# Performance work log

Measured on AMD Instinct MI355X. Metric: run time of the kernel, lower is better.

The kernel has to match this reference:

```python
import jax, jax.numpy as jnp
import numpy as np

N_NODES, N_EDGES, F_IN = 8192, 32768, 16
N_SUB, N_GRAPH = 512, 32
EDGE_DIM, HID = 5, 128
DIMS = [(16, 32), (32, 64), (64, 64)]  # (M_in, M_out) per NNConv layer


def _segment_mean(x, seg, n):
    s = jax.ops.segment_sum(x, seg, num_segments=n)
    c = jax.ops.segment_sum(jnp.ones((x.shape[0], 1), x.dtype), seg, num_segments=n)
    return s / jnp.maximum(c, 1.0)


def _nnconv(x, src, dst, eattr, W1, b1, W2, b2, root, bias):
    # edge MLP -> per-edge weight matrix theta: [E, M_in, M_out]
    h = jax.nn.relu(eattr @ W1 + b1)
    theta = (h @ W2 + b2).reshape(-1, x.shape[1], root.shape[1])
    msg = jnp.einsum('ei,eio->eo', x[src], theta)          # gather + per-edge matvec
    agg = jax.ops.segment_sum(msg, dst, num_segments=x.shape[0])  # scatter-add (aggr='add')
    return agg + x @ root + bias


def setup_inputs() -> dict:
    key = jax.random.key(0)
    ks = jax.random.split(key, 32)
    inp = {}
    inp['x'] = jax.random.normal(ks[0], (N_NODES, F_IN), jnp.float32)
    inp['edge_index'] = jax.random.randint(ks[1], (2, N_EDGES), 0, N_NODES)
    inp['edge_attr'] = jax.random.uniform(ks[2], (N_EDGES, EDGE_DIM), jnp.float32)
    inp['node_to_subgraph'] = jnp.sort(jax.random.randint(ks[3], (N_NODES,), 0, N_SUB))
    inp['subgraph_to_graph'] = jnp.sort(jax.random.randint(ks[4], (N_SUB,), 0, N_GRAPH))
    i = 5
    for l, (ci, co) in enumerate(DIMS):
        inp[f'W1_{l}'] = jax.random.normal(ks[i], (EDGE_DIM, HID), jnp.float32) * 0.1
        inp[f'b1_{l}'] = jnp.zeros((HID,), jnp.float32)
        inp[f'W2_{l}'] = jax.random.normal(ks[i + 1], (HID, ci * co), jnp.float32) * 0.05
        inp[f'b2_{l}'] = jnp.zeros((ci * co,), jnp.float32)
        inp[f'root_{l}'] = jax.random.normal(ks[i + 2], (ci, co), jnp.float32) * 0.1
        inp[f'bias_{l}'] = jnp.zeros((co,), jnp.float32)
        i += 3
    inp['fc1_w'] = jax.random.normal(ks[i], (64, 32), jnp.float32) * 0.1
    inp['fc1_b'] = jnp.zeros((32,), jnp.float32)
    inp['fc2_w'] = jax.random.normal(ks[i + 1], (32, 16), jnp.float32) * 0.1
    inp['fc2_b'] = jnp.zeros((16,), jnp.float32)
    inp['fc3_w'] = jax.random.normal(ks[i + 2], (16, 1), jnp.float32) * 0.1
    inp['fc3_b'] = jnp.zeros((1,), jnp.float32)
    return inp


def reference(x, edge_index, edge_attr, node_to_subgraph, subgraph_to_graph,
              W1_0, b1_0, W2_0, b2_0, root_0, bias_0,
              W1_1, b1_1, W2_1, b2_1, root_1, bias_1,
              W1_2, b1_2, W2_2, b2_2, root_2, bias_2,
              fc1_w, fc1_b, fc2_w, fc2_b, fc3_w, fc3_b):
    src, dst = edge_index[0], edge_index[1]
    layers = [(W1_0, b1_0, W2_0, b2_0, root_0, bias_0),
              (W1_1, b1_1, W2_1, b2_1, root_1, bias_1),
              (W1_2, b1_2, W2_2, b2_2, root_2, bias_2)]
    h = x
    for (W1, b1, W2, b2, root, bias) in layers:
        h = jax.nn.elu(_nnconv(h, src, dst, edge_attr, W1, b1, W2, b2, root, bias))
    h = _segment_mean(h, node_to_subgraph, N_SUB)      # global_mean_pool over subgraphs
    h = _segment_mean(h, subgraph_to_graph, N_GRAPH)   # global_mean_pool over graphs
    h = jax.nn.elu(h @ fc1_w + fc1_b)
    h = jax.nn.elu(h @ fc2_w + fc2_b)
    return (h @ fc3_w + fc3_b).reshape(-1)
```

## Files before the change

kernel.cpp:

```cpp
#include <hip/hip_runtime.h>

#define E_EDGES 32768
#define NN 8192
#define HID 128
#define KS 4

typedef _Float16 half8 __attribute__((ext_vector_type(8)));
typedef _Float16 half4 __attribute__((ext_vector_type(4)));
typedef float f32x4 __attribute__((ext_vector_type(4)));

__global__ void zero_init_k(int* __restrict__ hist, float* __restrict__ pools, int npool) {
  int t = blockIdx.x * 256 + threadIdx.x;
  if (t < NN) hist[t] = 0;
  if (t < npool) pools[t] = 0.f;
}

__global__ void hist_k(const int* __restrict__ dst, int* __restrict__ hist) {
  int e = blockIdx.x * 256 + threadIdx.x;
  if (e < E_EDGES) atomicAdd(&hist[dst[e]], 1);
}

__global__ void scan_k(const int* __restrict__ hist, int* __restrict__ roff, int* __restrict__ cursor) {
  __shared__ int ps[1024];
  int t = threadIdx.x;
  int loc[8]; int s = 0;
  int base = t * 8;
#pragma unroll
  for (int j = 0; j < 8; ++j) { loc[j] = s; s += hist[base + j]; }
  ps[t] = s;
  __syncthreads();
  for (int off = 1; off < 1024; off <<= 1) {
    int v = 0;
    if (t >= off) v = ps[t - off];
    __syncthreads();
    if (t >= off) ps[t] += v;
    __syncthreads();
  }
  int excl = (t == 0) ? 0 : ps[t - 1];
#pragma unroll
  for (int j = 0; j < 8; ++j) { int v = excl + loc[j]; roff[base + j] = v; cursor[base + j] = v; }
  if (t == 1023) roff[NN] = ps[1023];
}

__global__ void scatter_k(const int* __restrict__ dst, int* __restrict__ cursor, int* __restrict__ eidx) {
  int e = blockIdx.x * 256 + threadIdx.x;
  if (e < E_EDGES) { int p = atomicAdd(&cursor[dst[e]], 1); eidx[p] = e; }
}

template <int CI, int CO>
__device__ inline void prep_b_one(int idx, const float* __restrict__ W2,
                                  const float* __restrict__ b2, _Float16* __restrict__ out) {
  constexpr int Kmain = 128 * CI;
  constexpr int FC = CO / 16;
  int j = idx & 7;
  int h8 = idx >> 3;
  int lane = h8 & 63;
  int quad = lane >> 4, l15 = lane & 15;
  int rest = h8 >> 6;
  int fc = rest & (FC - 1);
  int c = rest / FC;
  int k = c * 32 + quad * 8 + j;
  int n = fc * 16 + l15;
  float v = 0.f;
  if (k < Kmain) v = W2[(size_t)k * CO + n];
  else if (k < Kmain + CI) v = b2[(k - Kmain) * CO + n];
  out[idx] = (_Float16)v;
}

__global__ void prep_b_all_k(const float* __restrict__ W2_0, const float* __restrict__ b2_0, _Float16* __restrict__ o0,
                             const float* __restrict__ W2_1, const float* __restrict__ b2_1, _Float16* __restrict__ o1,
                             const float* __restrict__ W2_2, const float* __restrict__ b2_2, _Float16* __restrict__ o2) {
  constexpr int N0 = 2176 * 32;
  constexpr int N1 = 4224 * 64;
  constexpr int N2 = 8320 * 64;
  int idx = blockIdx.x * 256 + threadIdx.x;
  if (idx < N0) prep_b_one<16, 32>(idx, W2_0, b2_0, o0);
  else if (idx < N0 + N1) prep_b_one<32, 64>(idx - N0, W2_1, b2_1, o1);
  else if (idx < N0 + N1 + N2) prep_b_one<64, 64>(idx - N0 - N1, W2_2, b2_2, o2);
}

__device__ inline half8 pack8(float4 a, float4 b) {
  half8 r;
  r[0] = (_Float16)a.x; r[1] = (_Float16)a.y; r[2] = (_Float16)a.z; r[3] = (_Float16)a.w;
  r[4] = (_Float16)b.x; r[5] = (_Float16)b.y; r[6] = (_Float16)b.z; r[7] = (_Float16)b.w;
  return r;
}

__device__ __forceinline__ void gload_lds16(const _Float16* g, _Float16* l) {
  __builtin_amdgcn_global_load_lds(
      (__attribute__((address_space(1))) void*)(size_t)(const void*)g,
      (__attribute__((address_space(3))) void*)(size_t)(void*)l, 16, 0, 0);
}

template <int CI, int CO>
__launch_bounds__(256, 2)
__global__ void msg_mfma_k(const float* __restrict__ xcur, const int* __restrict__ src,
                           const float* __restrict__ eattr, const float* __restrict__ W1,
                           const float* __restrict__ b1, const _Float16* __restrict__ Bsw,
                           float* __restrict__ msgbuf) {
  constexpr int ME = 256;
  constexpr int HSTR = 36;
  constexpr int FC = CO / 16;
  constexpr int NMAIN = CI / 4;
  constexpr int XPN = (CI == 64) ? 2 : 1;
  constexpr int RHALF = 4 * FC * 64 * 8;

  __shared__ _Float16 he_s[ME * HSTR];
  __shared__ float ea_s[ME * 5];
  __shared__ float W1s[5 * 32];
  __shared__ float b1s[32];
  __shared__ int src_s[ME];
  __shared__ _Float16 bls[2 * RHALF];

  int t = threadIdx.x;
  int e0 = blockIdx.x * ME;
  int y = blockIdx.y;
  int hbeg = y * 32;

  for (int j = t; j < ME * 5; j += 256) ea_s[j] = eattr[e0 * 5 + j];
  if (t < 5 * 32) W1s[t] = W1[(t >> 5) * HID + hbeg + (t & 31)];
  if (t < 32) b1s[t] = b1[hbeg + t];
  src_s[t] = src[e0 + t];
  __syncthreads();

  for (int j = t; j < 32 * ME; j += 256) {
    int hl = j & 31, e = j >> 5;
    float v = b1s[hl];
#pragma unroll
    for (int d = 0; d < 5; ++d) v += ea_s[e * 5 + d] * W1s[d * 32 + hl];
    he_s[e * HSTR + hl] = (_Float16)fmaxf(v, 0.f);
  }
  __syncthreads();

  int lane = t & 63;
  int w = t >> 6;
  int quad = lane >> 4, l15 = lane & 15;
  int qsh = (quad >> 1) << 4;
  int Rg0 = y * NMAIN;
  int NR = NMAIN + ((y == 3) ? 1 : 0);

  half8 xp[4][XPN];
  const _Float16* hbp[4];
#pragma unroll
  for (int fr = 0; fr < 4; ++fr) {
    int e = w * 64 + fr * 16 + l15;
    const float* xr = xcur + (size_t)src_s[e] * CI;
    int i0 = (CI == 16) ? ((quad & 1) * 8) : (quad * 8);
    float4 v0 = *(const float4*)(xr + i0);
    float4 v1 = *(const float4*)(xr + i0 + 4);
    xp[fr][0] = pack8(v0, v1);
    if constexpr (CI == 64) {
      float4 v2 = *(const float4*)(xr + i0 + 32);
      float4 v3 = *(const float4*)(xr + i0 + 36);
      xp[fr][1] = pack8(v2, v3);
    }
    hbp[fr] = he_s + e * HSTR;
  }

  f32x4 acc[4][FC];
#pragma unroll
  for (int fr = 0; fr < 4; ++fr)
#pragma unroll
    for (int fc = 0; fc < FC; ++fc)
#pragma unroll
      for (int r = 0; r < 4; ++r) acc[fr][fc][r] = 0.f;

  auto stageR = [&](int rg, int buf) {
    const _Float16* gb = Bsw + (size_t)rg * RHALF + w * (FC * 512);
    _Float16* lb = bls + buf * RHALF + w * (FC * 512);
#pragma unroll
    for (int i = 0; i < FC; ++i)
      gload_lds16(gb + i * 512 + lane * 8, lb + i * 512);
  };

  stageR(Rg0, 0);
  stageR(Rg0 + 1, 1);

  for (int r = 0; r < NR; ++r) {
    if (r + 1 < NR) {
      if constexpr (FC == 4) asm volatile("s_waitcnt vmcnt(4)" ::: "memory");
      else                   asm volatile("s_waitcnt vmcnt(2)" ::: "memory");
    } else {
      asm volatile("s_waitcnt vmcnt(0)" ::: "memory");
    }
    __builtin_amdgcn_s_barrier();

    const _Float16* bp = bls + (r & 1) * RHALF;
    int c0 = (Rg0 + r) * 4;

    if (r < NMAIN) {
      unsigned int hp2[4];
      half4 hp4[4];
      if constexpr (CI == 64) {
        int oh = (c0 >> 1) - hbeg;
#pragma unroll
        for (int fr = 0; fr < 4; ++fr) hp2[fr] = *(const unsigned int*)(hbp[fr] + oh);
      } else if constexpr (CI == 32) {
        int oh = c0 - hbeg;
#pragma unroll
        for (int fr = 0; fr < 4; ++fr) hp4[fr] = *(const half4*)(hbp[fr] + oh);
      }
#pragma unroll
      for (int cr = 0; cr < 4; ++cr) {
        int c = c0 + cr;
        half8 a[4];
#pragma unroll
        for (int fr = 0; fr < 4; ++fr) {
          if constexpr (CI == 64) {
            unsigned short hb = (unsigned short)((cr >= 2) ? (hp2[fr] >> 16) : hp2[fr]);
            _Float16 hv = __builtin_bit_cast(_Float16, hb);
            a[fr] = xp[fr][cr & 1] * hv;
          } else if constexpr (CI == 32) {
            a[fr] = xp[fr][0] * hp4[fr][cr];
          } else {
            unsigned int hw = *(const unsigned int*)(hbp[fr] + (2 * c - hbeg));
            _Float16 hv = __builtin_bit_cast(_Float16, (unsigned short)(hw >> qsh));
            a[fr] = xp[fr][0] * hv;
          }
        }
#pragma unroll
        for (int fc = 0; fc < FC; ++fc) {
          half8 bf = *(const half8*)&bp[((cr * FC + fc) * 64 + lane) * 8];
#pragma unroll
          for (int fr = 0; fr < 4; ++fr)
            acc[fr][fc] = __builtin_amdgcn_mfma_f32_16x16x32_f16(a[fr], bf, acc[fr][fc], 0, 0, 0);
        }
      }
    } else {
#pragma unroll
      for (int cr = 0; cr < 4; ++cr) {
        half8 a[4];
#pragma unroll
        for (int fr = 0; fr < 4; ++fr) a[fr] = xp[fr][(CI == 64) ? (cr & 1) : 0];
#pragma unroll
        for (int fc = 0; fc < FC; ++fc) {
          half8 bf = *(const half8*)&bp[((cr * FC + fc) * 64 + lane) * 8];
#pragma unroll
          for (int fr = 0; fr < 4; ++fr)
            acc[fr][fc] = __builtin_amdgcn_mfma_f32_16x16x32_f16(a[fr], bf, acc[fr][fc], 0, 0, 0);
        }
      }
    }

    asm volatile("s_waitcnt lgkmcnt(0)" ::: "memory");
    __builtin_amdgcn_s_barrier();
    if (r + 2 < NR) stageR(Rg0 + r + 2, r & 1);
  }

  float* mb = msgbuf + ((size_t)y * E_EDGES + e0) * CO;
#pragma unroll
  for (int fr = 0; fr < 4; ++fr)
#pragma unroll
    for (int fc = 0; fc < FC; ++fc)
#pragma unroll
      for (int r = 0; r < 4; ++r) {
        int el = w * 64 + fr * 16 + quad * 4 + r;
        int o = fc * 16 + l15;
        mb[el * CO + o] = acc[fr][fc][r];
      }
}

template <int CI, int CO, bool POOL>
__global__ void gather_elu_k(const float* __restrict__ xcur, const float* __restrict__ root,
                             const float* __restrict__ bias, const float* __restrict__ msgbuf,
                             const int* __restrict__ roff, const int* __restrict__ eidx,
                             float* __restrict__ xnext, const int* __restrict__ n2s,
                             float* __restrict__ ssum, float* __restrict__ scnt) {
  constexpr int NB = 256 / CO;
  __shared__ float xs[NB * CI];
  int t = threadIdx.x;
  int n0 = blockIdx.x * NB;
  for (int j = t; j < NB * CI; j += 256) xs[j] = xcur[n0 * CI + j];
  __syncthreads();
  int nl = t / CO, o = t & (CO - 1);
  int n = n0 + nl;
  float a = bias[o];
#pragma unroll
  for (int i = 0; i < CI; ++i) a += xs[nl * CI + i] * root[i * CO + o];
  int j1 = roff[n + 1];
  for (int j = roff[n]; j < j1; ++j) {
    int e = eidx[j];
    float m = 0.f;
#pragma unroll
    for (int s = 0; s < KS; ++s) m += msgbuf[((size_t)s * E_EDGES + e) * CO + o];
    a += m;
  }
  float v = a > 0.f ? a : expm1f(a);
  if constexpr (POOL) {
    int s = n2s[n];
    atomicAdd(&ssum[(s << 6) + o], v);
    if (o == 0) atomicAdd(&scnt[s], 1.f);
  } else {
    xnext[n * CO + o] = v;
  }
}

__global__ void pg_head_k(const float* __restrict__ ssum, const float* __restrict__ scnt,
                          const int* __restrict__ s2g,
                          const float* __restrict__ w1, const float* __restrict__ b1,
                          const float* __restrict__ w2, const float* __restrict__ b2,
                          const float* __restrict__ w3, const float* __restrict__ b3,
                          float* __restrict__ out) {
  int g = blockIdx.x;
  int t = threadIdx.x;
  __shared__ int s2s[512];
  __shared__ float hm[64], h1[32], h2[16];
  for (int i = t; i < 512; i += 64) s2s[i] = s2g[i];
  __syncthreads();
  float acc = 0.f, cnt = 0.f;
  for (int s = 0; s < 512; ++s) {
    if (s2s[s] == g) {
      acc += ssum[(s << 6) + t] / fmaxf(scnt[s], 1.f);
      cnt += 1.f;
    }
  }
  hm[t] = acc / fmaxf(cnt, 1.f);
  __syncthreads();
  if (t < 32) {
    float a = b1[t];
    for (int i = 0; i < 64; ++i) a += hm[i] * w1[i * 32 + t];
    h1[t] = a > 0.f ? a : expm1f(a);
  }
  __syncthreads();
  if (t < 16) {
    float a = b2[t];
    for (int i = 0; i < 32; ++i) a += h1[i] * w2[i * 16 + t];
    h2[t] = a > 0.f ? a : expm1f(a);
  }
  __syncthreads();
  if (t == 0) {
    float a = b3[0];
    for (int i = 0; i < 16; ++i) a += h2[i] * w3[i];
    out[g] = a;
  }
}

extern "C" void kernel_launch(void* const* d_in, const int* in_sizes, int n_in,
                              void* d_out, int out_size, void* d_ws, size_t ws_size,
                              hipStream_t stream) {
  (void)in_sizes; (void)n_in; (void)out_size; (void)ws_size;
  const float* x0 = (const float*)d_in[0];
  const int* ei = (const int*)d_in[1];
  const float* ea = (const float*)d_in[2];
  const int* n2s = (const int*)d_in[3];
  const int* s2g = (const int*)d_in[4];
  const float* W1_[3] = {(const float*)d_in[5], (const float*)d_in[11], (const float*)d_in[17]};
  const float* b1_[3] = {(const float*)d_in[6], (const float*)d_in[12], (const float*)d_in[18]};
  const float* W2_[3] = {(const float*)d_in[7], (const float*)d_in[13], (const float*)d_in[19]};
  const float* b2_[3] = {(const float*)d_in[8], (const float*)d_in[14], (const float*)d_in[20]};
  const float* rt_[3] = {(const float*)d_in[9], (const float*)d_in[15], (const float*)d_in[21]};
  const float* bs_[3] = {(const float*)d_in[10], (const float*)d_in[16], (const float*)d_in[22]};
  const float* fc1w = (const float*)d_in[23]; const float* fc1b = (const float*)d_in[24];
  const float* fc2w = (const float*)d_in[25]; const float* fc2b = (const float*)d_in[26];
  const float* fc3w = (const float*)d_in[27]; const float* fc3b = (const float*)d_in[28];
  float* out = (float*)d_out;

  const int* srcp = ei;
  const int* dstp = ei + E_EDGES;

  char* wsb = (char*)d_ws;
  size_t off = 0;
  auto alloc = [&](size_t bytes) {
    void* p = wsb + off;
    off += (bytes + 255) & ~(size_t)255;
    return p;
  };
  _Float16* Bsw0 = (_Float16*)alloc((size_t)2176 * 32 * 2);
  _Float16* Bsw1 = (_Float16*)alloc((size_t)4224 * 64 * 2);
  _Float16* Bsw2 = (_Float16*)alloc((size_t)8320 * 64 * 2);
  float* msgbuf = (float*)alloc((size_t)KS * E_EDGES * 64 * 4);
  float* x1 = (float*)alloc((size_t)NN * 32 * 4);
  float* x2 = (float*)alloc((size_t)NN * 64 * 4);
  int* hist = (int*)alloc((size_t)NN * 4);
  int* roff = (int*)alloc((size_t)(NN + 1) * 4);
  int* cursor = (int*)alloc((size_t)NN * 4);
  int* eidx = (int*)alloc((size_t)E_EDGES * 4);
  const int npool = 512 * 64 + 512;
  float* pools = (float*)alloc((size_t)npool * 4);
  float* ssum = pools;
  float* scnt = pools + 512 * 64;

  zero_init_k<<<(npool + 255) / 256, 256, 0, stream>>>(hist, pools, npool);
  hist_k<<<E_EDGES / 256, 256, 0, stream>>>(dstp, hist);
  scan_k<<<1, 1024, 0, stream>>>(hist, roff, cursor);
  scatter_k<<<E_EDGES / 256, 256, 0, stream>>>(dstp, cursor, eidx);
  prep_b_all_k<<<(2176 * 32 + 4224 * 64 + 8320 * 64) / 256, 256, 0, stream>>>(
      W2_[0], b2_[0], Bsw0, W2_[1], b2_[1], Bsw1, W2_[2], b2_[2], Bsw2);

  dim3 mg(E_EDGES / 256, KS);
  msg_mfma_k<16, 32><<<mg, 256, 0, stream>>>(x0, srcp, ea, W1_[0], b1_[0], Bsw0, msgbuf);
  gather_elu_k<16, 32, false><<<NN / 8, 256, 0, stream>>>(x0, rt_[0], bs_[0], msgbuf, roff, eidx, x1, nullptr, nullptr, nullptr);
  msg_mfma_k<32, 64><<<mg, 256, 0, stream>>>(x1, srcp, ea, W1_[1], b1_[1], Bsw1, msgbuf);
  gather_elu_k<32, 64, false><<<NN / 4, 256, 0, stream>>>(x1, rt_[1], bs_[1], msgbuf, roff, eidx, x2, nullptr, nullptr, nullptr);
  msg_mfma_k<64, 64><<<mg, 256, 0, stream>>>(x2, srcp, ea, W1_[2], b1_[2], Bsw2, msgbuf);
  gather_elu_k<64, 64, true><<<NN / 4, 256, 0, stream>>>(x2, rt_[2], bs_[2], msgbuf, roff, eidx, nullptr, n2s, ssum, scnt);

  pg_head_k<<<32, 64, 0, stream>>>(ssum, scnt, s2g, fc1w, fc1b, fc2w, fc2b, fc3w, fc3b, out);
}
```

Measured before the change: 278.3 us.

## Fuse zero-init into prep, shuffle scan, re-split MFMA waves, vectorize gather

Merges the buffer-zeroing kernel into the weight-swizzle prep kernel, which now writes eight halves per thread, and replaces the shared-memory Hillis-Steele scan with a wave-shuffle scan. Re-partitions the MFMA message kernel so each wave covers 128 edges and half of the output columns instead of 64 edges and all columns. This halves the LDS B-fragment reads per MFMA at the cost of more accumulator registers. The gather/ELU kernel now handles four outputs per thread with float4 loads and stores, cutting launch count and memory instructions.

```diff
diff --git a/kernel.cpp b/kernel.cpp
--- a/kernel.cpp
+++ b/kernel.cpp
@@ -9,37 +9,41 @@
 typedef _Float16 half4 __attribute__((ext_vector_type(4)));
 typedef float f32x4 __attribute__((ext_vector_type(4)));
 
-__global__ void zero_init_k(int* __restrict__ hist, float* __restrict__ pools, int npool) {
-  int t = blockIdx.x * 256 + threadIdx.x;
-  if (t < NN) hist[t] = 0;
-  if (t < npool) pools[t] = 0.f;
-}
-
 __global__ void hist_k(const int* __restrict__ dst, int* __restrict__ hist) {
   int e = blockIdx.x * 256 + threadIdx.x;
   if (e < E_EDGES) atomicAdd(&hist[dst[e]], 1);
 }
 
 __global__ void scan_k(const int* __restrict__ hist, int* __restrict__ roff, int* __restrict__ cursor) {
-  __shared__ int ps[1024];
+  __shared__ int wsum[16];
   int t = threadIdx.x;
+  int lane = t & 63, wv = t >> 6;
+  int base = t * 8;
   int loc[8]; int s = 0;
-  int base = t * 8;
 #pragma unroll
   for (int j = 0; j < 8; ++j) { loc[j] = s; s += hist[base + j]; }
-  ps[t] = s;
-  __syncthreads();
-  for (int off = 1; off < 1024; off <<= 1) {
-    int v = 0;
-    if (t >= off) v = ps[t - off];
-    __syncthreads();
-    if (t >= off) ps[t] += v;
-    __syncthreads();
-  }
-  int excl = (t == 0) ? 0 : ps[t - 1];
+  int inc = s;
+#pragma unroll
+  for (int off = 1; off < 64; off <<= 1) {
+    int u = __shfl_up(inc, off, 64);
+    if (lane >= off) inc += u;
+  }
+  if (lane == 63) wsum[wv] = inc;
+  __syncthreads();
+  if (t < 64) {
+    int u = (t < 16) ? wsum[t] : 0;
+#pragma unroll
+    for (int off = 1; off < 16; off <<= 1) {
+      int x = __shfl_up(u, off, 64);
+      if (lane >= off) u += x;
+    }
+    if (t < 16) wsum[t] = u;
+  }
+  __syncthreads();
+  int excl = (wv ? wsum[wv - 1] : 0) + inc - s;
 #pragma unroll
   for (int j = 0; j < 8; ++j) { int v = excl + loc[j]; roff[base + j] = v; cursor[base + j] = v; }
-  if (t == 1023) roff[NN] = ps[1023];
+  if (t == 1023) roff[NN] = wsum[15];
 }
 
 __global__ void scatter_k(const int* __restrict__ dst, int* __restrict__ cursor, int* __restrict__ eidx) {
@@ -48,35 +52,45 @@
 }
 
 template <int CI, int CO>
-__device__ inline void prep_b_one(int idx, const float* __restrict__ W2,
-                                  const float* __restrict__ b2, _Float16* __restrict__ out) {
+__device__ inline void prep8(int h8, const float* __restrict__ W2,
+                             const float* __restrict__ b2, _Float16* __restrict__ out) {
   constexpr int Kmain = 128 * CI;
   constexpr int FC = CO / 16;
-  int j = idx & 7;
-  int h8 = idx >> 3;
   int lane = h8 & 63;
   int quad = lane >> 4, l15 = lane & 15;
   int rest = h8 >> 6;
   int fc = rest & (FC - 1);
   int c = rest / FC;
-  int k = c * 32 + quad * 8 + j;
+  int k0 = c * 32 + quad * 8;
   int n = fc * 16 + l15;
-  float v = 0.f;
-  if (k < Kmain) v = W2[(size_t)k * CO + n];
-  else if (k < Kmain + CI) v = b2[(k - Kmain) * CO + n];
-  out[idx] = (_Float16)v;
-}
-
-__global__ void prep_b_all_k(const float* __restrict__ W2_0, const float* __restrict__ b2_0, _Float16* __restrict__ o0,
-                             const float* __restrict__ W2_1, const float* __restrict__ b2_1, _Float16* __restrict__ o1,
-                             const float* __restrict__ W2_2, const float* __restrict__ b2_2, _Float16* __restrict__ o2) {
-  constexpr int N0 = 2176 * 32;
-  constexpr int N1 = 4224 * 64;
-  constexpr int N2 = 8320 * 64;
-  int idx = blockIdx.x * 256 + threadIdx.x;
-  if (idx < N0) prep_b_one<16, 32>(idx, W2_0, b2_0, o0);
-  else if (idx < N0 + N1) prep_b_one<32, 64>(idx - N0, W2_1, b2_1, o1);
-  else if (idx < N0 + N1 + N2) prep_b_one<64, 64>(idx - N0 - N1, W2_2, b2_2, o2);
+  half8 r;
+#pragma unroll
+  for (int j = 0; j < 8; ++j) {
+    int k = k0 + j;
+    float v = 0.f;
+    if (k < Kmain) v = W2[(size_t)k * CO + n];
+    else if (k < Kmain + CI) v = b2[(k - Kmain) * CO + n];
+    r[j] = (_Float16)v;
+  }
+  *(half8*)(out + (size_t)h8 * 8) = r;
+}
+
+__global__ void prep_zero_k(const float* __restrict__ W2_0, const float* __restrict__ b2_0, _Float16* __restrict__ o0,
+                            const float* __restrict__ W2_1, const float* __restrict__ b2_1, _Float16* __restrict__ o1,
+                            const float* __restrict__ W2_2, const float* __restrict__ b2_2, _Float16* __restrict__ o2,
+                            int4* __restrict__ hist4, float4* __restrict__ pools4) {
+  constexpr int H0 = 2176 * 32 / 8;
+  constexpr int H1 = 4224 * 64 / 8;
+  constexpr int H2 = 8320 * 64 / 8;
+  constexpr int HT = H0 + H1 + H2;
+  constexpr int ZH = NN / 4;
+  constexpr int ZP = (512 * 64 + 512) / 4;
+  int tid = blockIdx.x * 256 + threadIdx.x;
+  if (tid < H0) prep8<16, 32>(tid, W2_0, b2_0, o0);
+  else if (tid < H0 + H1) prep8<32, 64>(tid - H0, W2_1, b2_1, o1);
+  else if (tid < HT) prep8<64, 64>(tid - H0 - H1, W2_2, b2_2, o2);
+  else if (tid < HT + ZH) hist4[tid - HT] = int4{0, 0, 0, 0};
+  else if (tid < HT + ZH + ZP) pools4[tid - HT - ZH] = float4{0.f, 0.f, 0.f, 0.f};
 }
 
 __device__ inline half8 pack8(float4 a, float4 b) {
@@ -101,6 +115,8 @@
   constexpr int ME = 256;
   constexpr int HSTR = 36;
   constexpr int FC = CO / 16;
+  constexpr int FCW = FC / 2;
+  constexpr int FR = 8;
   constexpr int NMAIN = CI / 4;
   constexpr int XPN = (CI == 64) ? 2 : 1;
   constexpr int RHALF = 4 * FC * 64 * 8;
@@ -134,16 +150,17 @@
 
   int lane = t & 63;
   int w = t >> 6;
+  int we = w & 1, wn = w >> 1;
   int quad = lane >> 4, l15 = lane & 15;
   int qsh = (quad >> 1) << 4;
   int Rg0 = y * NMAIN;
   int NR = NMAIN + ((y == 3) ? 1 : 0);
 
-  half8 xp[4][XPN];
-  const _Float16* hbp[4];
-#pragma unroll
-  for (int fr = 0; fr < 4; ++fr) {
-    int e = w * 64 + fr * 16 + l15;
+  half8 xp[FR][XPN];
+  int hoff[FR];
+#pragma unroll
+  for (int fr = 0; fr < FR; ++fr) {
+    int e = we * 128 + fr * 16 + l15;
     const float* xr = xcur + (size_t)src_s[e] * CI;
     int i0 = (CI == 16) ? ((quad & 1) * 8) : (quad * 8);
     float4 v0 = *(const float4*)(xr + i0);
@@ -154,14 +171,14 @@
       float4 v3 = *(const float4*)(xr + i0 + 36);
       xp[fr][1] = pack8(v2, v3);
     }
-    hbp[fr] = he_s + e * HSTR;
-  }
-
-  f32x4 acc[4][FC];
-#pragma unroll
-  for (int fr = 0; fr < 4; ++fr)
-#pragma unroll
-    for (int fc = 0; fc < FC; ++fc)
+    hoff[fr] = e * HSTR;
+  }
+
+  f32x4 acc[FR][FCW];
+#pragma unroll
+  for (int fr = 0; fr < FR; ++fr)
+#pragma unroll
+    for (int fc = 0; fc < FCW; ++fc)
 #pragma unroll
       for (int r = 0; r < 4; ++r) acc[fr][fc][r] = 0.f;
 
@@ -189,23 +206,23 @@
     int c0 = (Rg0 + r) * 4;
 
     if (r < NMAIN) {
-      unsigned int hp2[4];
-      half4 hp4[4];
+      unsigned int hp2[FR];
+      half4 hp4[FR];
       if constexpr (CI == 64) {
         int oh = (c0 >> 1) - hbeg;
 #pragma unroll
-        for (int fr = 0; fr < 4; ++fr) hp2[fr] = *(const unsigned int*)(hbp[fr] + oh);
+        for (int fr = 0; fr < FR; ++fr) hp2[fr] = *(const unsigned int*)(he_s + hoff[fr] + oh);
       } else if constexpr (CI == 32) {
         int oh = c0 - hbeg;
 #pragma unroll
-        for (int fr = 0; fr < 4; ++fr) hp4[fr] = *(const half4*)(hbp[fr] + oh);
+        for (int fr = 0; fr < FR; ++fr) hp4[fr] = *(const half4*)(he_s + hoff[fr] + oh);
       }
 #pragma unroll
       for (int cr = 0; cr < 4; ++cr) {
         int c = c0 + cr;
-        half8 a[4];
-#pragma unroll
-        for (int fr = 0; fr < 4; ++fr) {
+        half8 a[FR];
+#pragma unroll
+        for (int fr = 0; fr < FR; ++fr) {
           if constexpr (CI == 64) {
             unsigned short hb = (unsigned short)((cr >= 2) ? (hp2[fr] >> 16) : hp2[fr]);
             _Float16 hv = __builtin_bit_cast(_Float16, hb);
@@ -213,30 +230,30 @@
           } else if constexpr (CI == 32) {
             a[fr] = xp[fr][0] * hp4[fr][cr];
           } else {
-            unsigned int hw = *(const unsigned int*)(hbp[fr] + (2 * c - hbeg));
+            unsigned int hw = *(const unsigned int*)(he_s + hoff[fr] + (2 * c - hbeg));
             _Float16 hv = __builtin_bit_cast(_Float16, (unsigned short)(hw >> qsh));
             a[fr] = xp[fr][0] * hv;
           }
         }
 #pragma unroll
-        for (int fc = 0; fc < FC; ++fc) {
-          half8 bf = *(const half8*)&bp[((cr * FC + fc) * 64 + lane) * 8];
-#pragma unroll
-          for (int fr = 0; fr < 4; ++fr)
+        for (int fc = 0; fc < FCW; ++fc) {
+          half8 bf = *(const half8*)&bp[((cr * FC + wn * FCW + fc) * 64 + lane) * 8];
+#pragma unroll
+          for (int fr = 0; fr < FR; ++fr)
             acc[fr][fc] = __builtin_amdgcn_mfma_f32_16x16x32_f16(a[fr], bf, acc[fr][fc], 0, 0, 0);
         }
       }
     } else {
 #pragma unroll
       for (int cr = 0; cr < 4; ++cr) {
-        half8 a[4];
-#pragma unroll
-        for (int fr = 0; fr < 4; ++fr) a[fr] = xp[fr][(CI == 64) ? (cr & 1) : 0];
-#pragma unroll
-        for (int fc = 0; fc < FC; ++fc) {
-          half8 bf = *(const half8*)&bp[((cr * FC + fc) * 64 + lane) * 8];
-#pragma unroll
-          for (int fr = 0; fr < 4; ++fr)
+        half8 a[FR];
+#pragma unroll
+        for (int fr = 0; fr < FR; ++fr) a[fr] = xp[fr][(CI == 64) ? (cr & 1) : 0];
+#pragma unroll
+        for (int fc = 0; fc < FCW; ++fc) {
+          half8 bf = *(const half8*)&bp[((cr * FC + wn * FCW + fc) * 64 + lane) * 8];
+#pragma unroll
+          for (int fr = 0; fr < FR; ++fr)
             acc[fr][fc] = __builtin_amdgcn_mfma_f32_16x16x32_f16(a[fr], bf, acc[fr][fc], 0, 0, 0);
         }
       }
@@ -249,13 +266,13 @@
 
   float* mb = msgbuf + ((size_t)y * E_EDGES + e0) * CO;
 #pragma unroll
-  for (int fr = 0; fr < 4; ++fr)
-#pragma unroll
-    for (int fc = 0; fc < FC; ++fc)
+  for (int fr = 0; fr < FR; ++fr)
+#pragma unroll
+    for (int fc = 0; fc < FCW; ++fc)
 #pragma unroll
       for (int r = 0; r < 4; ++r) {
-        int el = w * 64 + fr * 16 + quad * 4 + r;
-        int o = fc * 16 + l15;
+        int el = we * 128 + fr * 16 + quad * 4 + r;
+        int o = (wn * FCW + fc) * 16 + l15;
         mb[el * CO + o] = acc[fr][fc][r];
       }
 }
@@ -266,32 +283,46 @@
                              const int* __restrict__ roff, const int* __restrict__ eidx,
                              float* __restrict__ xnext, const int* __restrict__ n2s,
                              float* __restrict__ ssum, float* __restrict__ scnt) {
-  constexpr int NB = 256 / CO;
+  constexpr int OV = CO / 4;
+  constexpr int NB = 256 / OV;
   __shared__ float xs[NB * CI];
   int t = threadIdx.x;
   int n0 = blockIdx.x * NB;
   for (int j = t; j < NB * CI; j += 256) xs[j] = xcur[n0 * CI + j];
   __syncthreads();
-  int nl = t / CO, o = t & (CO - 1);
+  int nl = t / OV, o4 = t & (OV - 1);
   int n = n0 + nl;
-  float a = bias[o];
-#pragma unroll
-  for (int i = 0; i < CI; ++i) a += xs[nl * CI + i] * root[i * CO + o];
+  float4 a = ((const float4*)bias)[o4];
+  const float4* root4 = (const float4*)root;
+#pragma unroll
+  for (int i = 0; i < CI; ++i) {
+    float xv = xs[nl * CI + i];
+    float4 rv = root4[i * OV + o4];
+    a.x += xv * rv.x; a.y += xv * rv.y; a.z += xv * rv.z; a.w += xv * rv.w;
+  }
   int j1 = roff[n + 1];
+  const float4* mb4 = (const float4*)msgbuf;
   for (int j = roff[n]; j < j1; ++j) {
     int e = eidx[j];
-    float m = 0.f;
-#pragma unroll
-    for (int s = 0; s < KS; ++s) m += msgbuf[((size_t)s * E_EDGES + e) * CO + o];
-    a += m;
-  }
-  float v = a > 0.f ? a : expm1f(a);
+#pragma unroll
+    for (int s = 0; s < KS; ++s) {
+      float4 m = mb4[((size_t)s * E_EDGES + e) * OV + o4];
+      a.x += m.x; a.y += m.y; a.z += m.z; a.w += m.w;
+    }
+  }
+  float4 v;
+  v.x = a.x > 0.f ? a.x : expm1f(a.x);
+  v.y = a.y > 0.f ? a.y : expm1f(a.y);
+  v.z = a.z > 0.f ? a.z : expm1f(a.z);
+  v.w = a.w > 0.f ? a.w : expm1f(a.w);
   if constexpr (POOL) {
     int s = n2s[n];
-    atomicAdd(&ssum[(s << 6) + o], v);
-    if (o == 0) atomicAdd(&scnt[s], 1.f);
+    float* sb = &ssum[(s << 6) + o4 * 4];
+    atomicAdd(sb + 0, v.x); atomicAdd(sb + 1, v.y);
+    atomicAdd(sb + 2, v.z); atomicAdd(sb + 3, v.w);
+    if (o4 == 0) atomicAdd(&scnt[s], 1.f);
   } else {
-    xnext[n * CO + o] = v;
+    ((float4*)xnext)[(size_t)n * OV + o4] = v;
   }
 }
 
@@ -380,20 +411,21 @@
   float* ssum = pools;
   float* scnt = pools + 512 * 64;
 
-  zero_init_k<<<(npool + 255) / 256, 256, 0, stream>>>(hist, pools, npool);
+  const int nprep = 109056 + 2048 + 8320;
+  prep_zero_k<<<(nprep + 255) / 256, 256, 0, stream>>>(
+      W2_[0], b2_[0], Bsw0, W2_[1], b2_[1], Bsw1, W2_[2], b2_[2], Bsw2,
+      (int4*)hist, (float4*)pools);
   hist_k<<<E_EDGES / 256, 256, 0, stream>>>(dstp, hist);
   scan_k<<<1, 1024, 0, stream>>>(hist, roff, cursor);
   scatter_k<<<E_EDGES / 256, 256, 0, stream>>>(dstp, cursor, eidx);
-  prep_b_all_k<<<(2176 * 32 + 4224 * 64 + 8320 * 64) / 256, 256, 0, stream>>>(
-      W2_[0], b2_[0], Bsw0, W2_[1], b2_[1], Bsw1, W2_[2], b2_[2], Bsw2);
 
   dim3 mg(E_EDGES / 256, KS);
   msg_mfma_k<16, 32><<<mg, 256, 0, stream>>>(x0, srcp, ea, W1_[0], b1_[0], Bsw0, msgbuf);
-  gather_elu_k<16, 32, false><<<NN / 8, 256, 0, stream>>>(x0, rt_[0], bs_[0], msgbuf, roff, eidx, x1, nullptr, nullptr, nullptr);
+  gather_elu_k<16, 32, false><<<NN / 32, 256, 0, stream>>>(x0, rt_[0], bs_[0], msgbuf, roff, eidx, x1, nullptr, nullptr, nullptr);
   msg_mfma_k<32, 64><<<mg, 256, 0, stream>>>(x1, srcp, ea, W1_[1], b1_[1], Bsw1, msgbuf);
-  gather_elu_k<32, 64, false><<<NN / 4, 256, 0, stream>>>(x1, rt_[1], bs_[1], msgbuf, roff, eidx, x2, nullptr, nullptr, nullptr);
+  gather_elu_k<32, 64, false><<<NN / 16, 256, 0, stream>>>(x1, rt_[1], bs_[1], msgbuf, roff, eidx, x2, nullptr, nullptr, nullptr);
   msg_mfma_k<64, 64><<<mg, 256, 0, stream>>>(x2, srcp, ea, W1_[2], b1_[2], Bsw2, msgbuf);
-  gather_elu_k<64, 64, true><<<NN / 4, 256, 0, stream>>>(x2, rt_[2], bs_[2], msgbuf, roff, eidx, nullptr, n2s, ssum, scnt);
+  gather_elu_k<64, 64, true><<<NN / 16, 256, 0, stream>>>(x2, rt_[2], bs_[2], msgbuf, roff, eidx, nullptr, n2s, ssum, scnt);
 
   pg_head_k<<<32, 64, 0, stream>>>(ssum, scnt, s2g, fc1w, fc1b, fc2w, fc2b, fc3w, fc3b, out);
 }
```

After: 287.1 us. 3.2% more time.
